# Performance work log

Measured on AMD Instinct MI355X. Metric: run time of the kernel, lower is better.

## Reference

```python
import jax, jax.numpy as jnp
import numpy as np

# ---- production-scale dims (see shape_source) ----
B, S = 256, 512            # batch, seq_len
HD, INTD = 512, 256        # hidden_dim, hidden_dim // dim_div
N_TEST, N_ITEM, N_TAG = 1500, 9454, 912
N_USER = 7442
GE_ROWS = N_USER + N_ITEM  # LightGCN table: users + items
N_CONT = 3


def _layer_norm(x, g, b, eps=1e-5):
    mu = jnp.mean(x, axis=-1, keepdims=True)
    var = jnp.var(x, axis=-1, keepdims=True)
    return (x - mu) * jax.lax.rsqrt(var + eps) * g + b


def setup_inputs() -> dict:
    key = jax.random.key(0)
    ks = jax.random.split(key, 14)
    f = lambda k, shp, s=0.02: jax.random.normal(k, shp, dtype=jnp.float32) * s
    return {
        # forward data args
        "cate_testId": jax.random.randint(ks[0], (B, S), 0, N_TEST),
        "cate_itemId": jax.random.randint(ks[1], (B, S), 0, N_ITEM),
        "cate_tag": jax.random.randint(ks[2], (B, S), 0, N_TAG),
        "cont_feats": jax.random.normal(ks[3], (B, S, N_CONT), dtype=jnp.float32),
        "interaction": jax.random.randint(ks[4], (B, S), 0, 3),
        # learned parameters
        "emb_interaction": f(ks[5], (3, INTD)),
        "emb_testId": f(ks[6], (N_TEST + 1, INTD)),
        "emb_itemId": f(ks[7], (N_ITEM + 1, INTD)),
        "emb_tag": f(ks[8], (N_TAG + 1, INTD)),
        "graph_table": f(ks[9], (GE_ROWS, HD)),           # pre-trained LightGCN embedding (np.load in torch)
        "graph_W": f(ks[10], (HD, INTD), 0.05),            # graph_linear (in, out) layout
        "graph_b": jnp.zeros((INTD,), jnp.float32),
        "comb_W": f(ks[11], (INTD * 5, HD // 2)),          # intd*(3 cate + 1 graph + interaction)
        "comb_b": jnp.zeros((HD // 2,), jnp.float32),
        "comb_g": jnp.ones((HD // 2,), jnp.float32),
        "comb_beta": jnp.zeros((HD // 2,), jnp.float32),
        "cont_W": f(ks[12], (N_CONT, HD // 2), 0.1),
        "cont_b": jnp.zeros((HD // 2,), jnp.float32),
        "cont_g": jnp.ones((HD // 2,), jnp.float32),
        "cont_beta": jnp.zeros((HD // 2,), jnp.float32),
    }


def reference(cate_testId, cate_itemId, cate_tag, cont_feats, interaction,
              emb_interaction, emb_testId, emb_itemId, emb_tag,
              graph_table, graph_W, graph_b,
              comb_W, comb_b, comb_g, comb_beta,
              cont_W, cont_b, cont_g, cont_beta):
    # categorical + interaction embedding lookups: [B,S,INTD] each
    e_int = emb_interaction[interaction]
    e_test = emb_testId[cate_testId]
    e_item = emb_itemId[cate_itemId]
    e_tag = emb_tag[cate_tag]
    # graph embedding path: fused gather (replaces the CPU python-loop gather)
    # indexes row (n_userID - 1 + value) of the LightGCN table, value from data[0]=testId
    g = graph_table[N_USER - 1 + cate_testId]          # [B,S,HD]
    g = g @ graph_W + graph_b                          # [B,S,INTD]
    embed = jnp.concatenate([e_int, e_test, e_item, e_tag, g], axis=-1)  # [B,S,5*INTD]
    cate = _layer_norm(embed @ comb_W + comb_b, comb_g, comb_beta)       # [B,S,HD//2]
    cont = _layer_norm(cont_feats @ cont_W + cont_b, cont_g, cont_beta)  # [B,S,HD//2]
    return jnp.concatenate([cate, cont], axis=-1)                        # [B,S,HD]
```

## Files before the change

kernel.cpp:

```cpp
#include <hip/hip_runtime.h>
#include <hip/hip_bf16.h>

#define NTOK   (256 * 512)
#define N_USER 7442

using bf16 = __hip_bfloat16;
typedef float f32x4 __attribute__((ext_vector_type(4)));

static __device__ __forceinline__ float4 ld4(const float* p) {
    return *reinterpret_cast<const float4*>(p);
}
static __device__ __forceinline__ float bfl(unsigned u) {
    union { unsigned u; float f; } c; c.u = u << 16; return c.f;
}
static __device__ __forceinline__ float bfh(unsigned u) {
    union { unsigned u; float f; } c; c.u = u & 0xFFFF0000u; return c.f;
}
static __device__ __forceinline__ void st_nt4(float* p, float x, float y, float z, float w) {
    f32x4 v; v.x = x; v.y = y; v.z = z; v.w = w;
    __builtin_nontemporal_store(v, reinterpret_cast<f32x4*>(p));
}
static __device__ __forceinline__ float rnd_bf(float x) {
    return __bfloat162float(__float2bfloat16(x));
}
static __device__ __forceinline__ void st_bf4(bf16* dst, float4 v) {
    union { bf16 h[4]; uint2 u; } pk;
    pk.h[0] = __float2bfloat16(v.x);
    pk.h[1] = __float2bfloat16(v.y);
    pk.h[2] = __float2bfloat16(v.z);
    pk.h[3] = __float2bfloat16(v.w);
    *reinterpret_cast<uint2*>(dst) = pk.u;
}

template <int CTRL, int ROW_MASK>
static __device__ __forceinline__ float dpp_add(float x) {
    const int sh = __builtin_amdgcn_update_dpp(0, __float_as_int(x), CTRL, ROW_MASK, 0xf, true);
    return x + __int_as_float(sh);
}
static __device__ __forceinline__ float wave_sum(float x) {
    x = dpp_add<0x111, 0xf>(x);
    x = dpp_add<0x112, 0xf>(x);
    x = dpp_add<0x114, 0xf>(x);
    x = dpp_add<0x118, 0xf>(x);
    x = dpp_add<0x142, 0xa>(x);
    x = dpp_add<0x143, 0xc>(x);
    return __int_as_float(__builtin_amdgcn_readlane(__float_as_int(x), 63));
}
static __device__ __forceinline__ float dot4(float4 a, float4 b) {
    return a.x * b.x + a.y * b.y + a.z * b.z + a.w * b.w;
}

#define RG  8
#define RSP 16
#define NB_TESTG 188
#define NB_ITEM  591
#define NB_TAG   58
#define NB_INT   1
#define NB_TOTAL (NB_TESTG + NB_ITEM + NB_TAG + NB_INT)

__global__ __launch_bounds__(256) void precompute_kernel(
    const float* __restrict__ emb_int,  const float* __restrict__ emb_test,
    const float* __restrict__ emb_item, const float* __restrict__ emb_tag,
    const float* __restrict__ graph_tab, const float* __restrict__ graph_W,
    const float* __restrict__ graph_b,
    const float* __restrict__ comb_W,   const float* __restrict__ comb_b,
    const float* __restrict__ cont_W,   const float* __restrict__ cont_b,
    bf16* __restrict__ Pint, bf16* __restrict__ Ptestg,
    bf16* __restrict__ Pitem, bf16* __restrict__ Ptag,
    float* __restrict__ Rint, float* __restrict__ Rtestg,
    float* __restrict__ Ritem, float* __restrict__ Rtag,
    float* __restrict__ CS) {
    __shared__ float lds[4096];
    const int tid  = threadIdx.x;
    const int w    = tid >> 6;
    const int lane = tid & 63;
    const int c    = lane * 4;
    const int b    = blockIdx.x;

    const float* W0 = comb_W;
    const float* W1 = comb_W + 256 * 256;
    const float* W2 = comb_W + 512 * 256;
    const float* W3 = comb_W + 768 * 256;
    const float* W4 = comb_W + 1024 * 256;

    if (b < NB_TESTG) {
        const int row0 = b * RG;
        const int nr   = min(RG, 1500 - row0);

        for (int i = tid; i < nr * 512; i += 256) {
            const int r = i >> 9, m = i & 511;
            lds[r * 512 + m] = graph_tab[(size_t)(N_USER - 1 + row0 + r) * 512 + m];
        }
        __syncthreads();

        float4 acc[2];
        acc[0] = float4{0.f, 0.f, 0.f, 0.f};
        acc[1] = float4{0.f, 0.f, 0.f, 0.f};
        for (int m = 0; m < 512; m += 4) {
            const float4 wv0 = ld4(graph_W + (m + 0) * 256 + c);
            const float4 wv1 = ld4(graph_W + (m + 1) * 256 + c);
            const float4 wv2 = ld4(graph_W + (m + 2) * 256 + c);
            const float4 wv3 = ld4(graph_W + (m + 3) * 256 + c);
            #pragma unroll
            for (int r = 0; r < 2; ++r) {
                const int rr = min(w * 2 + r, nr - 1);
                const float4 e = ld4(&lds[rr * 512 + m]);
                acc[r].x += e.x * wv0.x + e.y * wv1.x + e.z * wv2.x + e.w * wv3.x;
                acc[r].y += e.x * wv0.y + e.y * wv1.y + e.z * wv2.y + e.w * wv3.y;
                acc[r].z += e.x * wv0.z + e.y * wv1.z + e.z * wv2.z + e.w * wv3.z;
                acc[r].w += e.x * wv0.w + e.y * wv1.w + e.z * wv2.w + e.w * wv3.w;
            }
        }
        __syncthreads();

        #pragma unroll
        for (int r = 0; r < 2; ++r)
            *reinterpret_cast<float4*>(&lds[(w * 2 + r) * 256 + c]) = acc[r];
        for (int i = tid; i < nr * 256; i += 256) {
            const int r = i >> 8, m = i & 255;
            lds[2048 + r * 256 + m] = emb_test[(size_t)(row0 + r) * 256 + m];
        }
        __syncthreads();

        float4 acc2[2];
        float4 bacc = float4{0.f, 0.f, 0.f, 0.f};
        acc2[0] = float4{0.f, 0.f, 0.f, 0.f};
        acc2[1] = float4{0.f, 0.f, 0.f, 0.f};
        for (int m = 0; m < 256; m += 4) {
            const float4 w40 = ld4(W4 + (m + 0) * 256 + c);
            const float4 w41 = ld4(W4 + (m + 1) * 256 + c);
            const float4 w42 = ld4(W4 + (m + 2) * 256 + c);
            const float4 w43 = ld4(W4 + (m + 3) * 256 + c);
            const float4 w10 = ld4(W1 + (m + 0) * 256 + c);
            const float4 w11 = ld4(W1 + (m + 1) * 256 + c);
            const float4 w12 = ld4(W1 + (m + 2) * 256 + c);
            const float4 w13 = ld4(W1 + (m + 3) * 256 + c);
            const float gb0 = graph_b[m + 0], gb1 = graph_b[m + 1];
            const float gb2 = graph_b[m + 2], gb3 = graph_b[m + 3];
            bacc.x += gb0 * w40.x + gb1 * w41.x + gb2 * w42.x + gb3 * w43.x;
            bacc.y += gb0 * w40.y + gb1 * w41.y + gb2 * w42.y + gb3 * w43.y;
            bacc.z += gb0 * w40.z + gb1 * w41.z + gb2 * w42.z + gb3 * w43.z;
            bacc.w += gb0 * w40.w + gb1 * w41.w + gb2 * w42.w + gb3 * w43.w;
            #pragma unroll
            for (int r = 0; r < 2; ++r) {
                const int rr = min(w * 2 + r, nr - 1);
                const float4 tv = ld4(&lds[rr * 256 + m]);
                const float4 ev = ld4(&lds[2048 + rr * 256 + m]);
                acc2[r].x += tv.x * w40.x + tv.y * w41.x + tv.z * w42.x + tv.w * w43.x
                           + ev.x * w10.x + ev.y * w11.x + ev.z * w12.x + ev.w * w13.x;
                acc2[r].y += tv.x * w40.y + tv.y * w41.y + tv.z * w42.y + tv.w * w43.y
                           + ev.x * w10.y + ev.y * w11.y + ev.z * w12.y + ev.w * w13.y;
                acc2[r].z += tv.x * w40.z + tv.y * w41.z + tv.z * w42.z + tv.w * w43.z
                           + ev.x * w10.z + ev.y * w11.z + ev.z * w12.z + ev.w * w13.z;
                acc2[r].w += tv.x * w40.w + tv.y * w41.w + tv.z * w42.w + tv.w * w43.w
                           + ev.x * w10.w + ev.y * w11.w + ev.z * w12.w + ev.w * w13.w;
            }
        }
        const float4 cbv = ld4(comb_b + c);
        #pragma unroll
        for (int r = 0; r < 2; ++r) {
            const int row = w * 2 + r;
            float4 o;
            o.x = acc2[r].x + bacc.x + cbv.x;
            o.y = acc2[r].y + bacc.y + cbv.y;
            o.z = acc2[r].z + bacc.z + cbv.z;
            o.w = acc2[r].w + bacc.w + cbv.w;
            const float rs = wave_sum(rnd_bf(o.x) + rnd_bf(o.y) + rnd_bf(o.z) + rnd_bf(o.w));
            if (row < nr) {
                st_bf4(Ptestg + (size_t)(row0 + row) * 256 + c, o);
                if (lane == 0) Rtestg[row0 + row] = rs;
            }
        }
    } else {
        const float* E; const float* W; bf16* P; float* R; int row0, Rn;
        const int sb = b - NB_TESTG;
        const bool isInt = (sb >= NB_ITEM + NB_TAG);
        if (sb < NB_ITEM)               { E = emb_item; W = W2; P = Pitem; R = Ritem; row0 = sb * RSP;             Rn = 9455; }
        else if (sb < NB_ITEM + NB_TAG) { E = emb_tag;  W = W3; P = Ptag;  R = Rtag;  row0 = (sb - NB_ITEM) * RSP; Rn = 913;  }
        else                            { E = emb_int;  W = W0; P = Pint;  R = Rint;  row0 = 0;                    Rn = 3;    }
        const int nr = min(RSP, Rn - row0);

        for (int i = tid; i < nr * 256; i += 256) {
            const int r = i >> 8, m = i & 255;
            lds[r * 256 + m] = E[(size_t)(row0 + r) * 256 + m];
        }
        __syncthreads();

        if (w * 4 < nr) {
            float4 acc[4];
            #pragma unroll
            for (int r = 0; r < 4; ++r) acc[r] = float4{0.f, 0.f, 0.f, 0.f};
            for (int m = 0; m < 256; m += 4) {
                const float4 wv0 = ld4(W + (m + 0) * 256 + c);
                const float4 wv1 = ld4(W + (m + 1) * 256 + c);
                const float4 wv2 = ld4(W + (m + 2) * 256 + c);
                const float4 wv3 = ld4(W + (m + 3) * 256 + c);
                #pragma unroll
                for (int r = 0; r < 4; ++r) {
                    const int rr = min(w * 4 + r, nr - 1);
                    const float4 e = ld4(&lds[rr * 256 + m]);
                    acc[r].x += e.x * wv0.x + e.y * wv1.x + e.z * wv2.x + e.w * wv3.x;
                    acc[r].y += e.x * wv0.y + e.y * wv1.y + e.z * wv2.y + e.w * wv3.y;
                    acc[r].z += e.x * wv0.z + e.y * wv1.z + e.z * wv2.z + e.w * wv3.z;
                    acc[r].w += e.x * wv0.w + e.y * wv1.w + e.z * wv2.w + e.w * wv3.w;
                }
            }
            #pragma unroll
            for (int r = 0; r < 4; ++r) {
                const int row = w * 4 + r;
                const float rs = wave_sum(rnd_bf(acc[r].x) + rnd_bf(acc[r].y) +
                                          rnd_bf(acc[r].z) + rnd_bf(acc[r].w));
                if (row < nr) {
                    st_bf4(P + (size_t)(row0 + row) * 256 + c, acc[r]);
                    if (lane == 0) R[row0 + row] = rs;
                }
            }
        }

        if (isInt && w == 1) {
            const float4 a0 = ld4(cont_W + 0 * 256 + c);
            const float4 a1 = ld4(cont_W + 1 * 256 + c);
            const float4 a2 = ld4(cont_W + 2 * 256 + c);
            const float4 a3 = ld4(cont_b + c);
            const float inv256 = 1.f / 256.f;
            const float s0 = wave_sum(a0.x + a0.y + a0.z + a0.w) * inv256;
            const float s1 = wave_sum(a1.x + a1.y + a1.z + a1.w) * inv256;
            const float s2 = wave_sum(a2.x + a2.y + a2.z + a2.w) * inv256;
            const float s3 = wave_sum(a3.x + a3.y + a3.z + a3.w) * inv256;
            const float p00 = wave_sum(dot4(a0, a0)) * inv256;
            const float p11 = wave_sum(dot4(a1, a1)) * inv256;
            const float p22 = wave_sum(dot4(a2, a2)) * inv256;
            const float p33 = wave_sum(dot4(a3, a3)) * inv256;
            const float p01 = wave_sum(dot4(a0, a1)) * inv256;
            const float p02 = wave_sum(dot4(a0, a2)) * inv256;
            const float p12 = wave_sum(dot4(a1, a2)) * inv256;
            const float p03 = wave_sum(dot4(a0, a3)) * inv256;
            const float p13 = wave_sum(dot4(a1, a3)) * inv256;
            const float p23 = wave_sum(dot4(a2, a3)) * inv256;
            if (lane == 0) {
                CS[0] = s0;  CS[1] = s1;  CS[2] = s2;  CS[3] = s3;
                CS[4] = p00; CS[5] = p11; CS[6] = p22; CS[7] = p33;
                CS[8] = p01; CS[9] = p02; CS[10] = p12;
                CS[11] = p03; CS[12] = p13; CS[13] = p23;
                CS[14] = 0.f; CS[15] = 0.f;
            }
        }
    }
}

__global__ __launch_bounds__(256) void main_kernel(
    const int* __restrict__ testId, const int* __restrict__ itemId,
    const int* __restrict__ tagId,  const int* __restrict__ inter,
    const float* __restrict__ cont_feats,
    const bf16* __restrict__ Pint, const bf16* __restrict__ Ptestg,
    const bf16* __restrict__ Pitem, const bf16* __restrict__ Ptag,
    const float* __restrict__ Rint, const float* __restrict__ Rtestg,
    const float* __restrict__ Ritem, const float* __restrict__ Rtag,
    const float* __restrict__ CS,
    const float* __restrict__ comb_g, const float* __restrict__ comb_beta,
    const float* __restrict__ cont_W, const float* __restrict__ cont_b,
    const float* __restrict__ cont_g, const float* __restrict__ cont_beta,
    float* __restrict__ out) {
    const int wid  = blockIdx.x * 4 + (threadIdx.x >> 6);
    const int lane = threadIdx.x & 63;
    const int c    = lane * 4;

    const float4 g4  = ld4(comb_g + c);
    const float4 b4  = ld4(comb_beta + c);
    const float4 w0  = ld4(cont_W + 0 * 256 + c);
    const float4 w1  = ld4(cont_W + 1 * 256 + c);
    const float4 w2  = ld4(cont_W + 2 * 256 + c);
    const float4 cb  = ld4(cont_b + c);
    const float4 g42 = ld4(cont_g + c);
    const float4 b42 = ld4(cont_beta + c);
    const uint2 p0 = *reinterpret_cast<const uint2*>(Pint + 0 * 256 + c);
    const uint2 p1 = *reinterpret_cast<const uint2*>(Pint + 1 * 256 + c);
    const uint2 p2 = *reinterpret_cast<const uint2*>(Pint + 2 * 256 + c);
    const float ri0 = Rint[0], ri1 = Rint[1], ri2 = Rint[2];
    const float4 csA = ld4(CS + 0);
    const float4 csB = ld4(CS + 4);
    const float4 csC = ld4(CS + 8);
    const float4 csD = ld4(CS + 12);

    const int tb = wid * 4;
    const int4 tiv = *reinterpret_cast<const int4*>(testId + tb);
    const int4 iiv = *reinterpret_cast<const int4*>(itemId + tb);
    const int4 tgv = *reinterpret_cast<const int4*>(tagId  + tb);
    const int4 ivv = *reinterpret_cast<const int4*>(inter  + tb);
    const int tis[4] = {tiv.x, tiv.y, tiv.z, tiv.w};
    const int iis[4] = {iiv.x, iiv.y, iiv.z, iiv.w};
    const int tgs[4] = {tgv.x, tgv.y, tgv.z, tgv.w};
    const int ivs[4] = {ivv.x, ivv.y, ivv.z, ivv.w};
    const float4 cf0 = ld4(cont_feats + (size_t)tb * 3);
    const float4 cf1 = ld4(cont_feats + (size_t)tb * 3 + 4);
    const float4 cf2 = ld4(cont_feats + (size_t)tb * 3 + 8);
    const float cf[12] = {cf0.x, cf0.y, cf0.z, cf0.w,
                          cf1.x, cf1.y, cf1.z, cf1.w,
                          cf2.x, cf2.y, cf2.z, cf2.w};

    uint2 gT[4], gI[4], gG[4];
    float sT[4], sI[4], sG[4];
    #pragma unroll
    for (int j = 0; j < 4; ++j) {
        gT[j] = *reinterpret_cast<const uint2*>(Ptestg + (size_t)tis[j] * 256 + c);
        gI[j] = *reinterpret_cast<const uint2*>(Pitem  + (size_t)iis[j] * 256 + c);
        gG[j] = *reinterpret_cast<const uint2*>(Ptag   + (size_t)tgs[j] * 256 + c);
        sT[j] = Rtestg[tis[j]];
        sI[j] = Ritem[iis[j]];
        sG[j] = Rtag[tgs[j]];
    }

    #pragma unroll
    for (int j = 0; j < 4; ++j) {
        const int t = tb + j;

        uint2 u0;
        u0.x = ivs[j] == 0 ? p0.x : (ivs[j] == 1 ? p1.x : p2.x);
        u0.y = ivs[j] == 0 ? p0.y : (ivs[j] == 1 ? p1.y : p2.y);
        const float sInt = ivs[j] == 0 ? ri0 : (ivs[j] == 1 ? ri1 : ri2);

        const float vx = bfl(u0.x) + bfl(gT[j].x) + bfl(gI[j].x) + bfl(gG[j].x);
        const float vy = bfh(u0.x) + bfh(gT[j].x) + bfh(gI[j].x) + bfh(gG[j].x);
        const float vz = bfl(u0.y) + bfl(gT[j].y) + bfl(gI[j].y) + bfl(gG[j].y);
        const float vw = bfh(u0.y) + bfh(gT[j].y) + bfh(gI[j].y) + bfh(gG[j].y);

        const float s   = sInt + sT[j] + sI[j] + sG[j];
        const float ss  = wave_sum(vx * vx + vy * vy + vz * vz + vw * vw);
        const float mu  = s * (1.f / 256.f);
        const float var = ss * (1.f / 256.f) - mu * mu;
        const float inv = rsqrtf(var + 1e-5f);

        float* po = out + (size_t)t * 512;
        st_nt4(po + c,
               (vx - mu) * inv * g4.x + b4.x,
               (vy - mu) * inv * g4.y + b4.y,
               (vz - mu) * inv * g4.z + b4.z,
               (vw - mu) * inv * g4.w + b4.w);

        const float c0 = cf[j * 3 + 0];
        const float c1 = cf[j * 3 + 1];
        const float c2 = cf[j * 3 + 2];
        const float mu2 = c0 * csA.x + c1 * csA.y + c2 * csA.z + csA.w;
        const float e2  = c0 * c0 * csB.x + c1 * c1 * csB.y + c2 * c2 * csB.z + csB.w
                        + 2.f * (c0 * c1 * csC.x + c0 * c2 * csC.y + c1 * c2 * csC.z
                               + c0 * csC.w + c1 * csD.x + c2 * csD.y);
        const float var2 = e2 - mu2 * mu2;
        const float inv2 = rsqrtf(var2 + 1e-5f);

        const float ux = c0 * w0.x + c1 * w1.x + c2 * w2.x + cb.x;
        const float uy = c0 * w0.y + c1 * w1.y + c2 * w2.y + cb.y;
        const float uz = c0 * w0.z + c1 * w1.z + c2 * w2.z + cb.z;
        const float uw = c0 * w0.w + c1 * w1.w + c2 * w2.w + cb.w;

        st_nt4(po + 256 + c,
               (ux - mu2) * inv2 * g42.x + b42.x,
               (uy - mu2) * inv2 * g42.y + b42.y,
               (uz - mu2) * inv2 * g42.z + b42.z,
               (uw - mu2) * inv2 * g42.w + b42.w);
    }
}

extern "C" void kernel_launch(void* const* d_in, const int* in_sizes, int n_in,
                              void* d_out, int out_size, void* d_ws, size_t ws_size,
                              hipStream_t stream) {
    const int*   testId     = (const int*)d_in[0];
    const int*   itemId     = (const int*)d_in[1];
    const int*   tagId      = (const int*)d_in[2];
    const float* cont_feats = (const float*)d_in[3];
    const int*   inter      = (const int*)d_in[4];
    const float* emb_int    = (const float*)d_in[5];
    const float* emb_test   = (const float*)d_in[6];
    const float* emb_item   = (const float*)d_in[7];
    const float* emb_tag    = (const float*)d_in[8];
    const float* graph_tab  = (const float*)d_in[9];
    const float* graph_W    = (const float*)d_in[10];
    const float* graph_b    = (const float*)d_in[11];
    const float* comb_W     = (const float*)d_in[12];
    const float* comb_b     = (const float*)d_in[13];
    const float* comb_g     = (const float*)d_in[14];
    const float* comb_beta  = (const float*)d_in[15];
    const float* cont_W     = (const float*)d_in[16];
    const float* cont_b     = (const float*)d_in[17];
    const float* cont_g     = (const float*)d_in[18];
    const float* cont_beta  = (const float*)d_in[19];
    float* out              = (float*)d_out;

    bf16* ws     = (bf16*)d_ws;
    bf16* Pitem  = ws;
    bf16* Ptestg = Pitem  + 9455 * 256;
    bf16* Ptag   = Ptestg + 1500 * 256;
    bf16* Pint   = Ptag   +  913 * 256;
    float* Ritem  = (float*)(Pint + 3 * 256);
    float* Rtestg = Ritem  + 9455;
    float* Rtag   = Rtestg + 1500;
    float* Rint   = Rtag   +  913;
    float* CS     = Rint   + 3;

    precompute_kernel<<<NB_TOTAL, 256, 0, stream>>>(
        emb_int, emb_test, emb_item, emb_tag, graph_tab, graph_W, graph_b,
        comb_W, comb_b, cont_W, cont_b,
        Pint, Ptestg, Pitem, Ptag,
        Rint, Rtestg, Ritem, Rtag, CS);

    main_kernel<<<NTOK / (4 * 4), 256, 0, stream>>>(
        testId, itemId, tagId, inter, cont_feats,
        Pint, Ptestg, Pitem, Ptag,
        Rint, Rtestg, Ritem, Rtag, CS,
        comb_g, comb_beta, cont_W, cont_b, cont_g, cont_beta, out);
}
```

Baseline: 113.4 us.

## Move continuous-feature LayerNorm branch into precompute kernel to overlap with table precompute

Adds 2048 extra blocks to the precompute launch that compute the continuous-feature linear+LayerNorm half of the output directly, with the cont_W statistics computed per wave instead of staged through a workspace buffer. The main kernel now only writes the categorical half. The goal is to fill the GPU during the small precompute launch with independent output work and shrink the main kernel's register and store load. The cost is that every cont wave recomputes the 14 wave reductions, and the two kernels now write interleaved halves of each output row.

```diff
diff --git a/kernel.cpp b/kernel.cpp
--- a/kernel.cpp
+++ b/kernel.cpp
@@ -56,26 +56,92 @@
 #define NB_ITEM  591
 #define NB_TAG   58
 #define NB_INT   1
-#define NB_TOTAL (NB_TESTG + NB_ITEM + NB_TAG + NB_INT)
-
-__global__ __launch_bounds__(256) void precompute_kernel(
+#define NB_PC    (NB_TESTG + NB_ITEM + NB_TAG + NB_INT)
+#define NB_CONT  2048
+#define NB_A     (NB_PC + NB_CONT)
+
+__global__ __launch_bounds__(256) void precompute_cont_kernel(
     const float* __restrict__ emb_int,  const float* __restrict__ emb_test,
     const float* __restrict__ emb_item, const float* __restrict__ emb_tag,
     const float* __restrict__ graph_tab, const float* __restrict__ graph_W,
     const float* __restrict__ graph_b,
     const float* __restrict__ comb_W,   const float* __restrict__ comb_b,
+    const float* __restrict__ cont_feats,
     const float* __restrict__ cont_W,   const float* __restrict__ cont_b,
+    const float* __restrict__ cont_g,   const float* __restrict__ cont_beta,
     bf16* __restrict__ Pint, bf16* __restrict__ Ptestg,
     bf16* __restrict__ Pitem, bf16* __restrict__ Ptag,
     float* __restrict__ Rint, float* __restrict__ Rtestg,
     float* __restrict__ Ritem, float* __restrict__ Rtag,
-    float* __restrict__ CS) {
+    float* __restrict__ out) {
     __shared__ float lds[4096];
     const int tid  = threadIdx.x;
     const int w    = tid >> 6;
     const int lane = tid & 63;
     const int c    = lane * 4;
     const int b    = blockIdx.x;
+
+    if (b >= NB_PC) {
+        const float4 w0  = ld4(cont_W + 0 * 256 + c);
+        const float4 w1  = ld4(cont_W + 1 * 256 + c);
+        const float4 w2  = ld4(cont_W + 2 * 256 + c);
+        const float4 cb  = ld4(cont_b + c);
+        const float4 g42 = ld4(cont_g + c);
+        const float4 b42 = ld4(cont_beta + c);
+
+        const float inv256 = 1.f / 256.f;
+        const float M0  = wave_sum(w0.x + w0.y + w0.z + w0.w) * inv256;
+        const float M1  = wave_sum(w1.x + w1.y + w1.z + w1.w) * inv256;
+        const float M2  = wave_sum(w2.x + w2.y + w2.z + w2.w) * inv256;
+        const float M3  = wave_sum(cb.x + cb.y + cb.z + cb.w) * inv256;
+        const float P00 = wave_sum(dot4(w0, w0)) * inv256;
+        const float P11 = wave_sum(dot4(w1, w1)) * inv256;
+        const float P22 = wave_sum(dot4(w2, w2)) * inv256;
+        const float P33 = wave_sum(dot4(cb, cb)) * inv256;
+        const float P01 = wave_sum(dot4(w0, w1)) * inv256;
+        const float P02 = wave_sum(dot4(w0, w2)) * inv256;
+        const float P12 = wave_sum(dot4(w1, w2)) * inv256;
+        const float P03 = wave_sum(dot4(w0, cb)) * inv256;
+        const float P13 = wave_sum(dot4(w1, cb)) * inv256;
+        const float P23 = wave_sum(dot4(w2, cb)) * inv256;
+
+        const int wid = (b - NB_PC) * 4 + w;
+        const int t0  = wid * 16;
+        for (int k4 = 0; k4 < 4; ++k4) {
+            const int tb = t0 + k4 * 4;
+            const float4 cf0 = ld4(cont_feats + (size_t)tb * 3);
+            const float4 cf1 = ld4(cont_feats + (size_t)tb * 3 + 4);
+            const float4 cf2 = ld4(cont_feats + (size_t)tb * 3 + 8);
+            const float cf[12] = {cf0.x, cf0.y, cf0.z, cf0.w,
+                                  cf1.x, cf1.y, cf1.z, cf1.w,
+                                  cf2.x, cf2.y, cf2.z, cf2.w};
+            #pragma unroll
+            for (int j = 0; j < 4; ++j) {
+                const int t = tb + j;
+                const float c0 = cf[j * 3 + 0];
+                const float c1 = cf[j * 3 + 1];
+                const float c2 = cf[j * 3 + 2];
+                const float mu2 = c0 * M0 + c1 * M1 + c2 * M2 + M3;
+                const float e2  = c0 * c0 * P00 + c1 * c1 * P11 + c2 * c2 * P22 + P33
+                                + 2.f * (c0 * c1 * P01 + c0 * c2 * P02 + c1 * c2 * P12
+                                       + c0 * P03 + c1 * P13 + c2 * P23);
+                const float var2 = e2 - mu2 * mu2;
+                const float inv2 = rsqrtf(var2 + 1e-5f);
+
+                const float ux = c0 * w0.x + c1 * w1.x + c2 * w2.x + cb.x;
+                const float uy = c0 * w0.y + c1 * w1.y + c2 * w2.y + cb.y;
+                const float uz = c0 * w0.z + c1 * w1.z + c2 * w2.z + cb.z;
+                const float uw = c0 * w0.w + c1 * w1.w + c2 * w2.w + cb.w;
+
+                st_nt4(out + (size_t)t * 512 + 256 + c,
+                       (ux - mu2) * inv2 * g42.x + b42.x,
+                       (uy - mu2) * inv2 * g42.y + b42.y,
+                       (uz - mu2) * inv2 * g42.z + b42.z,
+                       (uw - mu2) * inv2 * g42.w + b42.w);
+            }
+        }
+        return;
+    }
 
     const float* W0 = comb_W;
     const float* W1 = comb_W + 256 * 256;
@@ -174,7 +240,6 @@
     } else {
         const float* E; const float* W; bf16* P; float* R; int row0, Rn;
         const int sb = b - NB_TESTG;
-        const bool isInt = (sb >= NB_ITEM + NB_TAG);
         if (sb < NB_ITEM)               { E = emb_item; W = W2; P = Pitem; R = Ritem; row0 = sb * RSP;             Rn = 9455; }
         else if (sb < NB_ITEM + NB_TAG) { E = emb_tag;  W = W3; P = Ptag;  R = Rtag;  row0 = (sb - NB_ITEM) * RSP; Rn = 913;  }
         else                            { E = emb_int;  W = W0; P = Pint;  R = Rint;  row0 = 0;                    Rn = 3;    }
@@ -216,71 +281,28 @@
                 }
             }
         }
-
-        if (isInt && w == 1) {
-            const float4 a0 = ld4(cont_W + 0 * 256 + c);
-            const float4 a1 = ld4(cont_W + 1 * 256 + c);
-            const float4 a2 = ld4(cont_W + 2 * 256 + c);
-            const float4 a3 = ld4(cont_b + c);
-            const float inv256 = 1.f / 256.f;
-            const float s0 = wave_sum(a0.x + a0.y + a0.z + a0.w) * inv256;
-            const float s1 = wave_sum(a1.x + a1.y + a1.z + a1.w) * inv256;
-            const float s2 = wave_sum(a2.x + a2.y + a2.z + a2.w) * inv256;
-            const float s3 = wave_sum(a3.x + a3.y + a3.z + a3.w) * inv256;
-            const float p00 = wave_sum(dot4(a0, a0)) * inv256;
-            const float p11 = wave_sum(dot4(a1, a1)) * inv256;
-            const float p22 = wave_sum(dot4(a2, a2)) * inv256;
-            const float p33 = wave_sum(dot4(a3, a3)) * inv256;
-            const float p01 = wave_sum(dot4(a0, a1)) * inv256;
-            const float p02 = wave_sum(dot4(a0, a2)) * inv256;
-            const float p12 = wave_sum(dot4(a1, a2)) * inv256;
-            const float p03 = wave_sum(dot4(a0, a3)) * inv256;
-            const float p13 = wave_sum(dot4(a1, a3)) * inv256;
-            const float p23 = wave_sum(dot4(a2, a3)) * inv256;
-            if (lane == 0) {
-                CS[0] = s0;  CS[1] = s1;  CS[2] = s2;  CS[3] = s3;
-                CS[4] = p00; CS[5] = p11; CS[6] = p22; CS[7] = p33;
-                CS[8] = p01; CS[9] = p02; CS[10] = p12;
-                CS[11] = p03; CS[12] = p13; CS[13] = p23;
-                CS[14] = 0.f; CS[15] = 0.f;
-            }
-        }
     }
 }
 
-__global__ __launch_bounds__(256) void main_kernel(
+__global__ __launch_bounds__(256) void main_cate_kernel(
     const int* __restrict__ testId, const int* __restrict__ itemId,
     const int* __restrict__ tagId,  const int* __restrict__ inter,
-    const float* __restrict__ cont_feats,
     const bf16* __restrict__ Pint, const bf16* __restrict__ Ptestg,
     const bf16* __restrict__ Pitem, const bf16* __restrict__ Ptag,
     const float* __restrict__ Rint, const float* __restrict__ Rtestg,
     const float* __restrict__ Ritem, const float* __restrict__ Rtag,
-    const float* __restrict__ CS,
     const float* __restrict__ comb_g, const float* __restrict__ comb_beta,
-    const float* __restrict__ cont_W, const float* __restrict__ cont_b,
-    const float* __restrict__ cont_g, const float* __restrict__ cont_beta,
     float* __restrict__ out) {
     const int wid  = blockIdx.x * 4 + (threadIdx.x >> 6);
     const int lane = threadIdx.x & 63;
     const int c    = lane * 4;
 
-    const float4 g4  = ld4(comb_g + c);
-    const float4 b4  = ld4(comb_beta + c);
-    const float4 w0  = ld4(cont_W + 0 * 256 + c);
-    const float4 w1  = ld4(cont_W + 1 * 256 + c);
-    const float4 w2  = ld4(cont_W + 2 * 256 + c);
-    const float4 cb  = ld4(cont_b + c);
-    const float4 g42 = ld4(cont_g + c);
-    const float4 b42 = ld4(cont_beta + c);
+    const float4 g4 = ld4(comb_g + c);
+    const float4 b4 = ld4(comb_beta + c);
     const uint2 p0 = *reinterpret_cast<const uint2*>(Pint + 0 * 256 + c);
     const uint2 p1 = *reinterpret_cast<const uint2*>(Pint + 1 * 256 + c);
     const uint2 p2 = *reinterpret_cast<const uint2*>(Pint + 2 * 256 + c);
     const float ri0 = Rint[0], ri1 = Rint[1], ri2 = Rint[2];
-    const float4 csA = ld4(CS + 0);
-    const float4 csB = ld4(CS + 4);
-    const float4 csC = ld4(CS + 8);
-    const float4 csD = ld4(CS + 12);
 
     const int tb = wid * 4;
     const int4 tiv = *reinterpret_cast<const int4*>(testId + tb);
@@ -291,12 +313,6 @@
     const int iis[4] = {iiv.x, iiv.y, iiv.z, iiv.w};
     const int tgs[4] = {tgv.x, tgv.y, tgv.z, tgv.w};
     const int ivs[4] = {ivv.x, ivv.y, ivv.z, ivv.w};
-    const float4 cf0 = ld4(cont_feats + (size_t)tb * 3);
-    const float4 cf1 = ld4(cont_feats + (size_t)tb * 3 + 4);
-    const float4 cf2 = ld4(cont_feats + (size_t)tb * 3 + 8);
-    const float cf[12] = {cf0.x, cf0.y, cf0.z, cf0.w,
-                          cf1.x, cf1.y, cf1.z, cf1.w,
-                          cf2.x, cf2.y, cf2.z, cf2.w};
 
     uint2 gT[4], gI[4], gG[4];
     float sT[4], sI[4], sG[4];
@@ -330,33 +346,11 @@
         const float var = ss * (1.f / 256.f) - mu * mu;
         const float inv = rsqrtf(var + 1e-5f);
 
-        float* po = out + (size_t)t * 512;
-        st_nt4(po + c,
+        st_nt4(out + (size_t)t * 512 + c,
                (vx - mu) * inv * g4.x + b4.x,
                (vy - mu) * inv * g4.y + b4.y,
                (vz - mu) * inv * g4.z + b4.z,
                (vw - mu) * inv * g4.w + b4.w);
-
-        const float c0 = cf[j * 3 + 0];
-        const float c1 = cf[j * 3 + 1];
-        const float c2 = cf[j * 3 + 2];
-        const float mu2 = c0 * csA.x + c1 * csA.y + c2 * csA.z + csA.w;
-        const float e2  = c0 * c0 * csB.x + c1 * c1 * csB.y + c2 * c2 * csB.z + csB.w
-                        + 2.f * (c0 * c1 * csC.x + c0 * c2 * csC.y + c1 * c2 * csC.z
-                               + c0 * csC.w + c1 * csD.x + c2 * csD.y);
-        const float var2 = e2 - mu2 * mu2;
-        const float inv2 = rsqrtf(var2 + 1e-5f);
-
-        const float ux = c0 * w0.x + c1 * w1.x + c2 * w2.x + cb.x;
-        const float uy = c0 * w0.y + c1 * w1.y + c2 * w2.y + cb.y;
-        const float uz = c0 * w0.z + c1 * w1.z + c2 * w2.z + cb.z;
-        const float uw = c0 * w0.w + c1 * w1.w + c2 * w2.w + cb.w;
-
-        st_nt4(po + 256 + c,
-               (ux - mu2) * inv2 * g42.x + b42.x,
-               (uy - mu2) * inv2 * g42.y + b42.y,
-               (uz - mu2) * inv2 * g42.z + b42.z,
-               (uw - mu2) * inv2 * g42.w + b42.w);
     }
 }
 
@@ -394,17 +388,16 @@
     float* Rtestg = Ritem  + 9455;
     float* Rtag   = Rtestg + 1500;
     float* Rint   = Rtag   +  913;
-    float* CS     = Rint   + 3;
-
-    precompute_kernel<<<NB_TOTAL, 256, 0, stream>>>(
+
+    precompute_cont_kernel<<<NB_A, 256, 0, stream>>>(
         emb_int, emb_test, emb_item, emb_tag, graph_tab, graph_W, graph_b,
-        comb_W, comb_b, cont_W, cont_b,
+        comb_W, comb_b, cont_feats, cont_W, cont_b, cont_g, cont_beta,
         Pint, Ptestg, Pitem, Ptag,
-        Rint, Rtestg, Ritem, Rtag, CS);
-
-    main_kernel<<<NTOK / (4 * 4), 256, 0, stream>>>(
-        testId, itemId, tagId, inter, cont_feats,
+        Rint, Rtestg, Ritem, Rtag, out);
+
+    main_cate_kernel<<<NTOK / (4 * 4), 256, 0, stream>>>(
+        testId, itemId, tagId, inter,
         Pint, Ptestg, Pitem, Ptag,
-        Rint, Rtestg, Ritem, Rtag, CS,
-        comb_g, comb_beta, cont_W, cont_b, cont_g, cont_beta, out);
-}
+        Rint, Rtestg, Ritem, Rtag,
+        comb_g, comb_beta, out);
+}
```

New measurement: 109.9 us. 3.0% less time.
